# Optimization experiments

Measured on AMD Instinct MI355X. Metric: run time of the kernel, lower is better.

Reference implementation:

```python
import jax, jax.numpy as jnp
import numpy as np

HIDDEN = 1024
STATE = 16
EXPAND = 2
INNER = HIDDEN * EXPAND
BATCH, SEQ = 4, 2048


def setup_inputs() -> dict:
    key = jax.random.key(0)
    ks = jax.random.split(key, 12)
    s = 0.02
    return {
        "x": jax.random.normal(ks[0], (BATCH, SEQ, HIDDEN), jnp.float32),
        "norm_scale": jnp.ones((HIDDEN,), jnp.float32),
        "norm_bias": jnp.zeros((HIDDEN,), jnp.float32),
        "W_in": jax.random.normal(ks[1], (HIDDEN, 2 * INNER), jnp.float32) * s,
        "conv_w": jax.random.normal(ks[2], (INNER, 3), jnp.float32) * 0.3,
        "conv_b": jnp.zeros((INNER,), jnp.float32),
        "W_dt": jax.random.normal(ks[3], (INNER, INNER), jnp.float32) * s,
        "b_dt": jnp.zeros((INNER,), jnp.float32),
        "A_log": jax.random.normal(ks[4], (INNER, STATE), jnp.float32),
        "D_param": jnp.ones((INNER,), jnp.float32),
        "W_B": jax.random.normal(ks[5], (INNER, STATE), jnp.float32) * s,
        "W_C": jax.random.normal(ks[6], (INNER, STATE), jnp.float32) * s,
        "W_out": jax.random.normal(ks[7], (INNER, HIDDEN), jnp.float32) * s,
    }


def reference(x, norm_scale, norm_bias, W_in, conv_w, conv_b, W_dt, b_dt,
              A_log, D_param, W_B, W_C, W_out):
    residual = x
    # LayerNorm (eps = 1e-5, matches nn.LayerNorm default)
    mu = jnp.mean(x, axis=-1, keepdims=True)
    var = jnp.mean(jnp.square(x - mu), axis=-1, keepdims=True)
    xn = (x - mu) * jax.lax.rsqrt(var + 1e-5) * norm_scale + norm_bias

    xz = xn @ W_in                         # [B, L, 2*inner]
    xb, z = jnp.split(xz, 2, axis=-1)      # each [B, L, inner]

    # depthwise conv1d, kernel 3, padding 1 (cross-correlation as in torch)
    xp = jnp.pad(xb, ((0, 0), (1, 1), (0, 0)))
    xb = (conv_w[:, 0] * xp[:, :-2] + conv_w[:, 1] * xp[:, 1:-1]
          + conv_w[:, 2] * xp[:, 2:] + conv_b)
    xb = jax.nn.silu(xb)

    dt = jax.nn.softplus(xb @ W_dt + b_dt)  # [B, L, inner]
    A = -jnp.exp(A_log)                     # [inner, N]
    Bi = xb @ W_B                           # [B, L, N]
    Ci = xb @ W_C                           # [B, L, N]

    def step(h, inp):
        x_t, dt_t, B_t, C_t = inp           # [B,D], [B,D], [B,N], [B,N]
        A_bar = jnp.exp(dt_t[:, :, None] * A)                 # [B, D, N]
        h = A_bar * h + (dt_t * x_t)[:, :, None] * B_t[:, None, :]
        y_t = jnp.einsum('bdn,bn->bd', h, C_t)
        return h, y_t

    h0 = jnp.zeros((x.shape[0], INNER, STATE), x.dtype)
    xs = (jnp.swapaxes(xb, 0, 1), jnp.swapaxes(dt, 0, 1),
          jnp.swapaxes(Bi, 0, 1), jnp.swapaxes(Ci, 0, 1))
    _, y = jax.lax.scan(step, h0, xs)       # y: [L, B, D]
    y = jnp.swapaxes(y, 0, 1)

    y = (y + D_param * xb) * jax.nn.silu(z)
    return residual + y @ W_out
```

## Files before the change

### kernel.cpp

```cpp
#include <hip/hip_runtime.h>
#include <hip/hip_bf16.h>
#include <cstdint>
#include <cstddef>

#define B_DIM 4
#define L_DIM 2048
#define H_DIM 1024
#define D_DIM 2048
#define N_STATE 16
#define TOKENS (B_DIM * L_DIM)
#define CH 32
#define LC (L_DIM / CH)
#define NEXT 2176

typedef __bf16 bf16x8 __attribute__((ext_vector_type(8)));
typedef float f32x4 __attribute__((ext_vector_type(4)));

__device__ __forceinline__ float sigmoidf_(float x) { return 1.f / (1.f + __expf(-x)); }
__device__ __forceinline__ float softplusf_(float x) {
  return fmaxf(x, 0.f) + log1pf(__expf(-fabsf(x)));
}
__device__ __forceinline__ void gl_lds16(const void* g, void* l) {
  __builtin_amdgcn_global_load_lds(
      (const __attribute__((address_space(1))) unsigned int*)g,
      (__attribute__((address_space(3))) unsigned int*)l, 16, 0, 0);
}

__device__ __forceinline__ void do_transpose(const float* __restrict__ in,
    __hip_bfloat16* __restrict__ out, int R, int C, int c0, int r0, int t) {
  __shared__ float tile[32][33];
  int tx = t & 31, ty = t >> 5;
  for (int i = 0; i < 32; i += 8)
    tile[ty + i][tx] = in[(size_t)(r0 + ty + i) * C + c0 + tx];
  __syncthreads();
  for (int i = 0; i < 32; i += 8)
    out[(size_t)(c0 + ty + i) * R + r0 + tx] = __float2bfloat16(tile[tx][ty + i]);
}

__global__ __launch_bounds__(256) void prep_kernel(
    const float* __restrict__ x, const float* __restrict__ gamma,
    const float* __restrict__ beta, __hip_bfloat16* __restrict__ xn,
    const float* __restrict__ W_in, __hip_bfloat16* __restrict__ W_inT,
    const float* __restrict__ W_dt, __hip_bfloat16* __restrict__ Wext,
    const float* __restrict__ WB, const float* __restrict__ WC) {
  int b = blockIdx.x;
  int t = threadIdx.x;
  if (b < TOKENS) {
    const float* px = x + (size_t)b * H_DIM;
    float4 v = *(const float4*)(px + t * 4);
    float s  = v.x + v.y + v.z + v.w;
    float ss = v.x * v.x + v.y * v.y + v.z * v.z + v.w * v.w;
    for (int off = 32; off > 0; off >>= 1) {
      s  += __shfl_down(s, off);
      ss += __shfl_down(ss, off);
    }
    __shared__ float red[8];
    __shared__ float stats[2];
    int wave = t >> 6, lane = t & 63;
    if (lane == 0) { red[wave] = s; red[4 + wave] = ss; }
    __syncthreads();
    if (t == 0) {
      float S  = red[0] + red[1] + red[2] + red[3];
      float SS = red[4] + red[5] + red[6] + red[7];
      float mu = S / H_DIM;
      float var = SS / H_DIM - mu * mu;
      stats[0] = mu;
      stats[1] = rsqrtf(var + 1e-5f);
    }
    __syncthreads();
    float mu = stats[0], rstd = stats[1];
    float4 g  = *(const float4*)(gamma + t * 4);
    float4 bt = *(const float4*)(beta + t * 4);
    __hip_bfloat16* po = xn + (size_t)b * H_DIM + t * 4;
    po[0] = __float2bfloat16((v.x - mu) * rstd * g.x + bt.x);
    po[1] = __float2bfloat16((v.y - mu) * rstd * g.y + bt.y);
    po[2] = __float2bfloat16((v.z - mu) * rstd * g.z + bt.z);
    po[3] = __float2bfloat16((v.w - mu) * rstd * g.w + bt.w);
    return;
  }
  b -= TOKENS;
  if (b < 4096) {
    do_transpose(W_in, W_inT, 1024, 4096, (b & 127) * 32, (b >> 7) * 32, t);
    return;
  }
  b -= 4096;
  if (b < 4096) {
    do_transpose(W_dt, Wext, 2048, 2048, (b & 63) * 32, (b >> 6) * 32, t);
    return;
  }
  b -= 4096;
  {
    int tid = b * 256 + t;
    int c = tid & 31;
    int k0 = (tid >> 5) * 16;
    const float* W = (c < 16) ? WB : WC;
    int cc = c & 15;
    __hip_bfloat16* o = Wext + (size_t)(2048 + c) * D_DIM + k0;
    for (int kk = 0; kk < 16; ++kk)
      o[kk] = __float2bfloat16(W[(size_t)(k0 + kk) * N_STATE + cc]);
  }
}

__global__ void transpose_bf16(const float* __restrict__ in,
                               __hip_bfloat16* __restrict__ out, int R, int C) {
  __shared__ float tile[32][33];
  int c0 = blockIdx.x * 32, r0 = blockIdx.y * 32;
  int tx = threadIdx.x, ty = threadIdx.y;
  for (int i = 0; i < 32; i += 8)
    tile[ty + i][tx] = in[(size_t)(r0 + ty + i) * C + c0 + tx];
  __syncthreads();
  for (int i = 0; i < 32; i += 8)
    out[(size_t)(c0 + ty + i) * R + r0 + tx] = __float2bfloat16(tile[tx][ty + i]);
}

#define BM 128
#define BN 128
#define BK 64

template <int MODE>
__global__ __launch_bounds__(256) void gemm_bf16(
    const __hip_bfloat16* __restrict__ A, const __hip_bfloat16* __restrict__ Bt,
    void* __restrict__ C0, void* __restrict__ C1, int nsplit,
    int K, int lda, int ldb, int ldc, int gx,
    const float* __restrict__ bias, const float* __restrict__ resid) {
  __shared__ __hip_bfloat16 As[2 * BM * BK];
  __shared__ __hip_bfloat16 Bs[2 * BN * BK];
  int t = threadIdx.x;
  int bid = blockIdx.x;
  int nsup = gx << 3;
  int super = bid / nsup;
  int rem = bid - super * nsup;
  int m0 = (super * 8 + (rem & 7)) * BM;
  int n0 = (rem >> 3) * BN;

  int wave = t >> 6, lane = t & 63;
  int quad = lane >> 4, l16 = lane & 15;
  int wm = (wave >> 1) * 64, wn = (wave & 1) * 64;

  f32x4 acc[4][4] = {};

  int srow  = t >> 3;
  int cslot = t & 7;
  int cdata = cslot ^ (srow & 7);
  const __hip_bfloat16* Ag[4];
  const __hip_bfloat16* Bg[4];
  int soff[4];
#pragma unroll
  for (int j = 0; j < 4; ++j) {
    Ag[j]  = A  + (size_t)(m0 + j * 32 + srow) * lda + cdata * 8;
    Bg[j]  = Bt + (size_t)(n0 + j * 32 + srow) * ldb + cdata * 8;
    soff[j] = (j * 32 + srow) * BK + cslot * 8;
  }

  const int NT = K / BK;
#pragma unroll
  for (int j = 0; j < 4; ++j) {
    gl_lds16(Ag[j], &As[soff[j]]);
    gl_lds16(Bg[j], &Bs[soff[j]]);
  }
  asm volatile("s_waitcnt vmcnt(0)" ::: "memory");
  __builtin_amdgcn_s_barrier();

  for (int kt = 0; kt < NT; ++kt) {
    const int cur = (kt & 1) * (BM * BK);
    const int nxt = cur ^ (BM * BK);
    if (kt + 1 < NT) {
      const int k1 = (kt + 1) * BK;
#pragma unroll
      for (int j = 0; j < 4; ++j) {
        gl_lds16(Ag[j] + k1, &As[nxt + soff[j]]);
        gl_lds16(Bg[j] + k1, &Bs[nxt + soff[j]]);
      }
    }
#pragma unroll
    for (int s = 0; s < 2; ++s) {
      int cs = ((s * 4 + quad) ^ (l16 & 7)) * 8;
      bf16x8 af[4], bf_[4];
#pragma unroll
      for (int i = 0; i < 4; ++i) {
        af[i]  = *(const bf16x8*)&As[cur + (wm + i * 16 + l16) * BK + cs];
        bf_[i] = *(const bf16x8*)&Bs[cur + (wn + i * 16 + l16) * BK + cs];
      }
#pragma unroll
      for (int i = 0; i < 4; ++i)
#pragma unroll
        for (int j = 0; j < 4; ++j)
          acc[i][j] = __builtin_amdgcn_mfma_f32_16x16x32_bf16(af[i], bf_[j], acc[i][j], 0, 0, 0);
    }
    asm volatile("s_waitcnt vmcnt(0)" ::: "memory");
    __builtin_amdgcn_s_barrier();
  }

#pragma unroll
  for (int i = 0; i < 4; ++i) {
    int row0 = m0 + wm + i * 16 + quad * 4;
#pragma unroll
    for (int j = 0; j < 4; ++j) {
      int col = n0 + wn + j * 16 + l16;
      f32x4 v = acc[i][j];
      if (MODE == 0) {
#pragma unroll
        for (int r = 0; r < 4; ++r) {
          size_t idx = (size_t)(row0 + r) * ldc + col;
          ((float*)C0)[idx] = v[r] + resid[idx];
        }
      } else if (MODE == 1) {
        bool mainc = (col < nsplit);
        __hip_bfloat16* cb = mainc ? (__hip_bfloat16*)C0 : (__hip_bfloat16*)C1;
        int ccol = mainc ? col : col - nsplit;
#pragma unroll
        for (int r = 0; r < 4; ++r)
          cb[(size_t)(row0 + r) * ldc + ccol] = __float2bfloat16(v[r]);
      } else {
        if (col < nsplit) {
          float bb = bias[col];
#pragma unroll
          for (int r = 0; r < 4; ++r)
            ((__hip_bfloat16*)C0)[(size_t)(row0 + r) * ldc + col] =
                __float2bfloat16(softplusf_(v[r] + bb));
        } else {
#pragma unroll
          for (int r = 0; r < 4; ++r)
            ((float*)C1)[(size_t)(row0 + r) * 128 + (col - nsplit)] = v[r];
        }
      }
    }
  }
}

__global__ __launch_bounds__(256) void conv_silu_kernel(const __hip_bfloat16* __restrict__ xb,
    const float* __restrict__ cw, const float* __restrict__ cb,
    __hip_bfloat16* __restrict__ xbc) {
  size_t i2 = (size_t)blockIdx.x * 256 + threadIdx.x;
  int dp = (int)(i2 & (D_DIM / 2 - 1));
  size_t tok = i2 >> 10;
  int l = (int)(tok & (L_DIM - 1));
  int d = dp * 2;
  const __hip_bfloat162* base = (const __hip_bfloat162*)xb + i2;
  __hip_bfloat162 cc = base[0];
  float v0 = cw[d * 3 + 1] * __bfloat162float(cc.x) + cb[d];
  float v1 = cw[d * 3 + 4] * __bfloat162float(cc.y) + cb[d + 1];
  if (l > 0) {
    __hip_bfloat162 pm = base[-(D_DIM / 2)];
    v0 += cw[d * 3 + 0] * __bfloat162float(pm.x);
    v1 += cw[d * 3 + 3] * __bfloat162float(pm.y);
  }
  if (l < L_DIM - 1) {
    __hip_bfloat162 pp = base[D_DIM / 2];
    v0 += cw[d * 3 + 2] * __bfloat162float(pp.x);
    v1 += cw[d * 3 + 5] * __bfloat162float(pp.y);
  }
  v0 = v0 * sigmoidf_(v0);
  v1 = v1 * sigmoidf_(v1);
  __hip_bfloat162 o;
  o.x = __float2bfloat16(v0);
  o.y = __float2bfloat16(v1);
  ((__hip_bfloat162*)xbc)[i2] = o;
}

__global__ __launch_bounds__(256) void scan1_kernel(const __hip_bfloat16* __restrict__ dt,
    const __hip_bfloat16* __restrict__ xbc, const float* __restrict__ BiCi,
    const float* __restrict__ A_log, float* __restrict__ hfin,
    float* __restrict__ dtsum) {
  __shared__ float Bsh[LC * N_STATE];
  int t = threadIdx.x;
  int d = blockIdx.x * 256 + t;
  int c = blockIdx.y, b = blockIdx.z;
  size_t base = (size_t)b * L_DIM + (size_t)c * LC;
  for (int idx = t; idx < LC * 4; idx += 256) {
    int row = idx >> 2, q = idx & 3;
    ((float4*)Bsh)[row * 4 + q] = *(const float4*)&BiCi[(base + row) * 128 + q * 4];
  }
  float Aneg[N_STATE];
  {
    const float4* Ap = (const float4*)(A_log + (size_t)d * N_STATE);
#pragma unroll
    for (int q = 0; q < 4; ++q) {
      float4 av = Ap[q];
      Aneg[4 * q + 0] = -__expf(av.x);
      Aneg[4 * q + 1] = -__expf(av.y);
      Aneg[4 * q + 2] = -__expf(av.z);
      Aneg[4 * q + 3] = -__expf(av.w);
    }
  }
  __syncthreads();
  const __hip_bfloat16* dtp = dt + base * D_DIM + d;
  const __hip_bfloat16* xp = xbc + base * D_DIM + d;
  float h[N_STATE];
#pragma unroll
  for (int n = 0; n < N_STATE; ++n) h[n] = 0.f;
  float ds = 0.f;
  float dtv = __bfloat162float(dtp[0]), xv = __bfloat162float(xp[0]);
  for (int i = 0; i < LC; ++i) {
    int ip = (i < LC - 1) ? i + 1 : i;
    float dt2 = __bfloat162float(dtp[(size_t)ip * D_DIM]);
    float x2  = __bfloat162float(xp[(size_t)ip * D_DIM]);
    float dtx = dtv * xv;
    ds += dtv;
    const float4* Brow = (const float4*)&Bsh[i * N_STATE];
#pragma unroll
    for (int q = 0; q < 4; ++q) {
      float4 bv = Brow[q];
      h[4*q+0] = __expf(dtv * Aneg[4*q+0]) * h[4*q+0] + dtx * bv.x;
      h[4*q+1] = __expf(dtv * Aneg[4*q+1]) * h[4*q+1] + dtx * bv.y;
      h[4*q+2] = __expf(dtv * Aneg[4*q+2]) * h[4*q+2] + dtx * bv.z;
      h[4*q+3] = __expf(dtv * Aneg[4*q+3]) * h[4*q+3] + dtx * bv.w;
    }
    dtv = dt2; xv = x2;
  }
  float* ho = hfin + (((size_t)b * CH + c) * D_DIM + d) * N_STATE;
#pragma unroll
  for (int q = 0; q < 4; ++q) {
    float4 v; v.x = h[4*q]; v.y = h[4*q+1]; v.z = h[4*q+2]; v.w = h[4*q+3];
    ((float4*)ho)[q] = v;
  }
  dtsum[((size_t)b * CH + c) * D_DIM + d] = ds;
}

__global__ __launch_bounds__(256) void scan2_kernel(const float* __restrict__ hfin,
    const float* __restrict__ dtsum, const float* __restrict__ A_log,
    float* __restrict__ hstart) {
  int tid = blockIdx.x * 256 + threadIdx.x;
  int n = tid & 15;
  int d = (tid >> 4) & (D_DIM - 1);
  int b = tid >> 15;
  float Aneg = -__expf(A_log[d * N_STATE + n]);
  float run = 0.f;
  for (int c = 0; c < CH; ++c) {
    size_t o = (((size_t)b * CH + c) * D_DIM + d) * N_STATE + n;
    hstart[o] = run;
    run = __expf(Aneg * dtsum[((size_t)b * CH + c) * D_DIM + d]) * run + hfin[o];
  }
}

__global__ __launch_bounds__(256) void scan3_kernel(const __hip_bfloat16* __restrict__ dt,
    const __hip_bfloat16* __restrict__ xbc, const float* __restrict__ BiCi,
    const float* __restrict__ A_log,
    const float* __restrict__ hstart, const __hip_bfloat16* __restrict__ z,
    const float* __restrict__ Dp, __hip_bfloat16* __restrict__ yo) {
  __shared__ float Bsh[LC * N_STATE];
  __shared__ float Csh[LC * N_STATE];
  int t = threadIdx.x;
  int d = blockIdx.x * 256 + t;
  int c = blockIdx.y, b = blockIdx.z;
  size_t base = (size_t)b * L_DIM + (size_t)c * LC;
  for (int idx = t; idx < LC * 4; idx += 256) {
    int row = idx >> 2, q = idx & 3;
    ((float4*)Bsh)[row * 4 + q] = *(const float4*)&BiCi[(base + row) * 128 + q * 4];
    ((float4*)Csh)[row * 4 + q] = *(const float4*)&BiCi[(base + row) * 128 + 16 + q * 4];
  }
  float Aneg[N_STATE];
  {
    const float4* Ap = (const float4*)(A_log + (size_t)d * N_STATE);
#pragma unroll
    for (int q = 0; q < 4; ++q) {
      float4 av = Ap[q];
      Aneg[4 * q + 0] = -__expf(av.x);
      Aneg[4 * q + 1] = -__expf(av.y);
      Aneg[4 * q + 2] = -__expf(av.z);
      Aneg[4 * q + 3] = -__expf(av.w);
    }
  }
  float h[N_STATE];
  {
    const float4* hs = (const float4*)(hstart + (((size_t)b * CH + c) * D_DIM + d) * N_STATE);
#pragma unroll
    for (int q = 0; q < 4; ++q) {
      float4 v = hs[q];
      h[4*q] = v.x; h[4*q+1] = v.y; h[4*q+2] = v.z; h[4*q+3] = v.w;
    }
  }
  float Dv = Dp[d];
  __syncthreads();
  const __hip_bfloat16* dtp = dt + base * D_DIM + d;
  const __hip_bfloat16* xp = xbc + base * D_DIM + d;
  const __hip_bfloat16* zp = z + base * D_DIM + d;
  __hip_bfloat16* yp = yo + base * D_DIM + d;
  float dtv = __bfloat162float(dtp[0]), xv = __bfloat162float(xp[0]);
  float zv = __bfloat162float(zp[0]);
  for (int i = 0; i < LC; ++i) {
    int ip = (i < LC - 1) ? i + 1 : i;
    float dt2 = __bfloat162float(dtp[(size_t)ip * D_DIM]);
    float x2  = __bfloat162float(xp[(size_t)ip * D_DIM]);
    float z2  = __bfloat162float(zp[(size_t)ip * D_DIM]);
    float dtx = dtv * xv;
    const float4* Brow = (const float4*)&Bsh[i * N_STATE];
    const float4* Crow = (const float4*)&Csh[i * N_STATE];
    float yv = 0.f;
#pragma unroll
    for (int q = 0; q < 4; ++q) {
      float4 bv = Brow[q];
      float4 cv = Crow[q];
      h[4*q+0] = __expf(dtv * Aneg[4*q+0]) * h[4*q+0] + dtx * bv.x;
      h[4*q+1] = __expf(dtv * Aneg[4*q+1]) * h[4*q+1] + dtx * bv.y;
      h[4*q+2] = __expf(dtv * Aneg[4*q+2]) * h[4*q+2] + dtx * bv.z;
      h[4*q+3] = __expf(dtv * Aneg[4*q+3]) * h[4*q+3] + dtx * bv.w;
      yv += h[4*q+0] * cv.x + h[4*q+1] * cv.y + h[4*q+2] * cv.z + h[4*q+3] * cv.w;
    }
    float g = zv * sigmoidf_(zv);
    yp[(size_t)i * D_DIM] = __float2bfloat16((yv + Dv * xv) * g);
    dtv = dt2; xv = x2; zv = z2;
  }
}

extern "C" void kernel_launch(void* const* d_in, const int* in_sizes, int n_in,
                              void* d_out, int out_size, void* d_ws, size_t ws_size,
                              hipStream_t stream) {
  const float* x          = (const float*)d_in[0];
  const float* norm_scale = (const float*)d_in[1];
  const float* norm_bias  = (const float*)d_in[2];
  const float* W_in       = (const float*)d_in[3];
  const float* conv_w     = (const float*)d_in[4];
  const float* conv_b     = (const float*)d_in[5];
  const float* W_dt       = (const float*)d_in[6];
  const float* b_dt       = (const float*)d_in[7];
  const float* A_log      = (const float*)d_in[8];
  const float* D_param    = (const float*)d_in[9];
  const float* W_B        = (const float*)d_in[10];
  const float* W_C        = (const float*)d_in[11];
  const float* W_out      = (const float*)d_in[12];
  float* out = (float*)d_out;

  const size_t MB = 1024 * 1024;
  const size_t NEEDED = 193 * MB;
  if (ws_size < NEEDED) return;

  char* ws = (char*)d_ws;
  __hip_bfloat16* xn     = (__hip_bfloat16*)(ws);
  __hip_bfloat16* W_outT = (__hip_bfloat16*)(ws);
  __hip_bfloat16* xb     = (__hip_bfloat16*)(ws + 16 * MB);
  __hip_bfloat16* ybf    = (__hip_bfloat16*)(ws + 16 * MB);
  __hip_bfloat16* z      = (__hip_bfloat16*)(ws + 48 * MB);
  __hip_bfloat16* xbc    = (__hip_bfloat16*)(ws + 80 * MB);
  __hip_bfloat16* dtY    = (__hip_bfloat16*)(ws + 112 * MB);
  float*          BiCi   = (float*)(ws + 144 * MB);
  __hip_bfloat16* W_ext  = (__hip_bfloat16*)(ws + 148 * MB);
  float*          hstart = (float*)(ws + 158 * MB);
  float*          dtsum  = (float*)(ws + 174 * MB);
  __hip_bfloat16* W_inT  = (__hip_bfloat16*)(ws + 177 * MB);
  float*          hfin   = (float*)(ws + 177 * MB);

  prep_kernel<<<TOKENS + 4096 + 4096 + 16, 256, 0, stream>>>(
      x, norm_scale, norm_bias, xn, W_in, W_inT, W_dt, W_ext, W_B, W_C);
  gemm_bf16<1><<<(4096 / BN) * (TOKENS / BM), 256, 0, stream>>>(
      xn, W_inT, xb, z, D_DIM, H_DIM, H_DIM, H_DIM, D_DIM, 4096 / BN,
      nullptr, nullptr);
  dim3 tb(32, 8);
  transpose_bf16<<<dim3(1024 / 32, 2048 / 32), tb, 0, stream>>>(W_out, W_outT, 2048, 1024);
  conv_silu_kernel<<<(TOKENS * D_DIM / 2) / 256, 256, 0, stream>>>(xb, conv_w, conv_b, xbc);
  gemm_bf16<2><<<(NEXT / BN) * (TOKENS / BM), 256, 0, stream>>>(
      xbc, W_ext, dtY, BiCi, D_DIM, D_DIM, D_DIM, D_DIM, D_DIM, NEXT / BN,
      b_dt, nullptr);
  scan1_kernel<<<dim3(D_DIM / 256, CH, B_DIM), 256, 0, stream>>>(
      dtY, xbc, BiCi, A_log, hfin, dtsum);
  scan2_kernel<<<(B_DIM * D_DIM * N_STATE) / 256, 256, 0, stream>>>(
      hfin, dtsum, A_log, hstart);
  scan3_kernel<<<dim3(D_DIM / 256, CH, B_DIM), 256, 0, stream>>>(
      dtY, xbc, BiCi, A_log, hstart, z, D_param, ybf);
  gemm_bf16<0><<<(H_DIM / BN) * (TOKENS / BM), 256, 0, stream>>>(
      ybf, W_outT, out, nullptr, 1 << 30, D_DIM, D_DIM, D_DIM, H_DIM, H_DIM / BN,
      nullptr, x);
}
```

Baseline: 571.8 us.

## Replace three-pass chunked scan with single sequential per-state scan kernel

```diff
diff --git a/kernel.cpp b/kernel.cpp
--- a/kernel.cpp
+++ b/kernel.cpp
@@ -9,8 +9,6 @@
 #define D_DIM 2048
 #define N_STATE 16
 #define TOKENS (B_DIM * L_DIM)
-#define CH 32
-#define LC (L_DIM / CH)
 #define NEXT 2176
 
 typedef __bf16 bf16x8 __attribute__((ext_vector_type(8)));
@@ -258,148 +256,49 @@
   ((__hip_bfloat162*)xbc)[i2] = o;
 }
 
-__global__ __launch_bounds__(256) void scan1_kernel(const __hip_bfloat16* __restrict__ dt,
-    const __hip_bfloat16* __restrict__ xbc, const float* __restrict__ BiCi,
-    const float* __restrict__ A_log, float* __restrict__ hfin,
-    float* __restrict__ dtsum) {
-  __shared__ float Bsh[LC * N_STATE];
+__global__ __launch_bounds__(256) void scan_fused(
+    const __hip_bfloat16* __restrict__ dt, const __hip_bfloat16* __restrict__ xbc,
+    const float* __restrict__ BiCi, const float* __restrict__ A_log,
+    const __hip_bfloat16* __restrict__ z, const float* __restrict__ Dp,
+    __hip_bfloat16* __restrict__ yo) {
   int t = threadIdx.x;
-  int d = blockIdx.x * 256 + t;
-  int c = blockIdx.y, b = blockIdx.z;
-  size_t base = (size_t)b * L_DIM + (size_t)c * LC;
-  for (int idx = t; idx < LC * 4; idx += 256) {
-    int row = idx >> 2, q = idx & 3;
-    ((float4*)Bsh)[row * 4 + q] = *(const float4*)&BiCi[(base + row) * 128 + q * 4];
-  }
-  float Aneg[N_STATE];
-  {
-    const float4* Ap = (const float4*)(A_log + (size_t)d * N_STATE);
-#pragma unroll
-    for (int q = 0; q < 4; ++q) {
-      float4 av = Ap[q];
-      Aneg[4 * q + 0] = -__expf(av.x);
-      Aneg[4 * q + 1] = -__expf(av.y);
-      Aneg[4 * q + 2] = -__expf(av.z);
-      Aneg[4 * q + 3] = -__expf(av.w);
-    }
-  }
-  __syncthreads();
-  const __hip_bfloat16* dtp = dt + base * D_DIM + d;
-  const __hip_bfloat16* xp = xbc + base * D_DIM + d;
-  float h[N_STATE];
-#pragma unroll
-  for (int n = 0; n < N_STATE; ++n) h[n] = 0.f;
-  float ds = 0.f;
-  float dtv = __bfloat162float(dtp[0]), xv = __bfloat162float(xp[0]);
-  for (int i = 0; i < LC; ++i) {
-    int ip = (i < LC - 1) ? i + 1 : i;
-    float dt2 = __bfloat162float(dtp[(size_t)ip * D_DIM]);
-    float x2  = __bfloat162float(xp[(size_t)ip * D_DIM]);
-    float dtx = dtv * xv;
-    ds += dtv;
-    const float4* Brow = (const float4*)&Bsh[i * N_STATE];
-#pragma unroll
-    for (int q = 0; q < 4; ++q) {
-      float4 bv = Brow[q];
-      h[4*q+0] = __expf(dtv * Aneg[4*q+0]) * h[4*q+0] + dtx * bv.x;
-      h[4*q+1] = __expf(dtv * Aneg[4*q+1]) * h[4*q+1] + dtx * bv.y;
-      h[4*q+2] = __expf(dtv * Aneg[4*q+2]) * h[4*q+2] + dtx * bv.z;
-      h[4*q+3] = __expf(dtv * Aneg[4*q+3]) * h[4*q+3] + dtx * bv.w;
-    }
-    dtv = dt2; xv = x2;
-  }
-  float* ho = hfin + (((size_t)b * CH + c) * D_DIM + d) * N_STATE;
-#pragma unroll
-  for (int q = 0; q < 4; ++q) {
-    float4 v; v.x = h[4*q]; v.y = h[4*q+1]; v.z = h[4*q+2]; v.w = h[4*q+3];
-    ((float4*)ho)[q] = v;
-  }
-  dtsum[((size_t)b * CH + c) * D_DIM + d] = ds;
-}
-
-__global__ __launch_bounds__(256) void scan2_kernel(const float* __restrict__ hfin,
-    const float* __restrict__ dtsum, const float* __restrict__ A_log,
-    float* __restrict__ hstart) {
-  int tid = blockIdx.x * 256 + threadIdx.x;
-  int n = tid & 15;
-  int d = (tid >> 4) & (D_DIM - 1);
-  int b = tid >> 15;
-  float Aneg = -__expf(A_log[d * N_STATE + n]);
-  float run = 0.f;
-  for (int c = 0; c < CH; ++c) {
-    size_t o = (((size_t)b * CH + c) * D_DIM + d) * N_STATE + n;
-    hstart[o] = run;
-    run = __expf(Aneg * dtsum[((size_t)b * CH + c) * D_DIM + d]) * run + hfin[o];
-  }
-}
-
-__global__ __launch_bounds__(256) void scan3_kernel(const __hip_bfloat16* __restrict__ dt,
-    const __hip_bfloat16* __restrict__ xbc, const float* __restrict__ BiCi,
-    const float* __restrict__ A_log,
-    const float* __restrict__ hstart, const __hip_bfloat16* __restrict__ z,
-    const float* __restrict__ Dp, __hip_bfloat16* __restrict__ yo) {
-  __shared__ float Bsh[LC * N_STATE];
-  __shared__ float Csh[LC * N_STATE];
-  int t = threadIdx.x;
-  int d = blockIdx.x * 256 + t;
-  int c = blockIdx.y, b = blockIdx.z;
-  size_t base = (size_t)b * L_DIM + (size_t)c * LC;
-  for (int idx = t; idx < LC * 4; idx += 256) {
-    int row = idx >> 2, q = idx & 3;
-    ((float4*)Bsh)[row * 4 + q] = *(const float4*)&BiCi[(base + row) * 128 + q * 4];
-    ((float4*)Csh)[row * 4 + q] = *(const float4*)&BiCi[(base + row) * 128 + 16 + q * 4];
-  }
-  float Aneg[N_STATE];
-  {
-    const float4* Ap = (const float4*)(A_log + (size_t)d * N_STATE);
-#pragma unroll
-    for (int q = 0; q < 4; ++q) {
-      float4 av = Ap[q];
-      Aneg[4 * q + 0] = -__expf(av.x);
-      Aneg[4 * q + 1] = -__expf(av.y);
-      Aneg[4 * q + 2] = -__expf(av.z);
-      Aneg[4 * q + 3] = -__expf(av.w);
-    }
-  }
-  float h[N_STATE];
-  {
-    const float4* hs = (const float4*)(hstart + (((size_t)b * CH + c) * D_DIM + d) * N_STATE);
-#pragma unroll
-    for (int q = 0; q < 4; ++q) {
-      float4 v = hs[q];
-      h[4*q] = v.x; h[4*q+1] = v.y; h[4*q+2] = v.z; h[4*q+3] = v.w;
-    }
-  }
+  int n = t & 15;
+  int dl = t >> 4;
+  int b = blockIdx.x >> 7;
+  int d = ((blockIdx.x & 127) << 4) + dl;
+  float Aneg = -__expf(A_log[(size_t)d * N_STATE + n]);
   float Dv = Dp[d];
-  __syncthreads();
-  const __hip_bfloat16* dtp = dt + base * D_DIM + d;
-  const __hip_bfloat16* xp = xbc + base * D_DIM + d;
-  const __hip_bfloat16* zp = z + base * D_DIM + d;
-  __hip_bfloat16* yp = yo + base * D_DIM + d;
-  float dtv = __bfloat162float(dtp[0]), xv = __bfloat162float(xp[0]);
-  float zv = __bfloat162float(zp[0]);
-  for (int i = 0; i < LC; ++i) {
-    int ip = (i < LC - 1) ? i + 1 : i;
+  size_t tb = (size_t)b * L_DIM;
+  const __hip_bfloat16* dtp = dt + tb * D_DIM + d;
+  const __hip_bfloat16* xp  = xbc + tb * D_DIM + d;
+  const __hip_bfloat16* zp  = z + tb * D_DIM + d;
+  const float* bp = BiCi + tb * 128 + n;
+  __hip_bfloat16* yp = yo + tb * D_DIM + d;
+
+  float h = 0.f;
+  float dtv = __bfloat162float(dtp[0]);
+  float xv  = __bfloat162float(xp[0]);
+  float zv  = __bfloat162float(zp[0]);
+  float bv  = bp[0];
+  float cv  = bp[16];
+  for (int i = 0; i < L_DIM; ++i) {
+    int ip = (i < L_DIM - 1) ? i + 1 : i;
     float dt2 = __bfloat162float(dtp[(size_t)ip * D_DIM]);
     float x2  = __bfloat162float(xp[(size_t)ip * D_DIM]);
     float z2  = __bfloat162float(zp[(size_t)ip * D_DIM]);
-    float dtx = dtv * xv;
-    const float4* Brow = (const float4*)&Bsh[i * N_STATE];
-    const float4* Crow = (const float4*)&Csh[i * N_STATE];
-    float yv = 0.f;
-#pragma unroll
-    for (int q = 0; q < 4; ++q) {
-      float4 bv = Brow[q];
-      float4 cv = Crow[q];
-      h[4*q+0] = __expf(dtv * Aneg[4*q+0]) * h[4*q+0] + dtx * bv.x;
-      h[4*q+1] = __expf(dtv * Aneg[4*q+1]) * h[4*q+1] + dtx * bv.y;
-      h[4*q+2] = __expf(dtv * Aneg[4*q+2]) * h[4*q+2] + dtx * bv.z;
-      h[4*q+3] = __expf(dtv * Aneg[4*q+3]) * h[4*q+3] + dtx * bv.w;
-      yv += h[4*q+0] * cv.x + h[4*q+1] * cv.y + h[4*q+2] * cv.z + h[4*q+3] * cv.w;
-    }
-    float g = zv * sigmoidf_(zv);
-    yp[(size_t)i * D_DIM] = __float2bfloat16((yv + Dv * xv) * g);
-    dtv = dt2; xv = x2; zv = z2;
+    float b2  = bp[(size_t)ip * 128];
+    float c2  = bp[(size_t)ip * 128 + 16];
+    h = __expf(dtv * Aneg) * h + (dtv * xv) * bv;
+    float p = h * cv;
+    p += __shfl_xor(p, 1);
+    p += __shfl_xor(p, 2);
+    p += __shfl_xor(p, 4);
+    p += __shfl_xor(p, 8);
+    if (n == 0) {
+      float g = zv * sigmoidf_(zv);
+      yp[(size_t)i * D_DIM] = __float2bfloat16((p + Dv * xv) * g);
+    }
+    dtv = dt2; xv = x2; zv = z2; bv = b2; cv = c2;
   }
 }
 
@@ -435,10 +334,7 @@
   __hip_bfloat16* dtY    = (__hip_bfloat16*)(ws + 112 * MB);
   float*          BiCi   = (float*)(ws + 144 * MB);
   __hip_bfloat16* W_ext  = (__hip_bfloat16*)(ws + 148 * MB);
-  float*          hstart = (float*)(ws + 158 * MB);
-  float*          dtsum  = (float*)(ws + 174 * MB);
   __hip_bfloat16* W_inT  = (__hip_bfloat16*)(ws + 177 * MB);
-  float*          hfin   = (float*)(ws + 177 * MB);
 
   prep_kernel<<<TOKENS + 4096 + 4096 + 16, 256, 0, stream>>>(
       x, norm_scale, norm_bias, xn, W_in, W_inT, W_dt, W_ext, W_B, W_C);
@@ -451,12 +347,8 @@
   gemm_bf16<2><<<(NEXT / BN) * (TOKENS / BM), 256, 0, stream>>>(
       xbc, W_ext, dtY, BiCi, D_DIM, D_DIM, D_DIM, D_DIM, D_DIM, NEXT / BN,
       b_dt, nullptr);
-  scan1_kernel<<<dim3(D_DIM / 256, CH, B_DIM), 256, 0, stream>>>(
-      dtY, xbc, BiCi, A_log, hfin, dtsum);
-  scan2_kernel<<<(B_DIM * D_DIM * N_STATE) / 256, 256, 0, stream>>>(
-      hfin, dtsum, A_log, hstart);
-  scan3_kernel<<<dim3(D_DIM / 256, CH, B_DIM), 256, 0, stream>>>(
-      dtY, xbc, BiCi, A_log, hstart, z, D_param, ybf);
+  scan_fused<<<B_DIM * (D_DIM / 16), 256, 0, stream>>>(
+      dtY, xbc, BiCi, A_log, z, D_param, ybf);
   gemm_bf16<0><<<(H_DIM / BN) * (TOKENS / BM), 256, 0, stream>>>(
       ybf, W_outT, out, nullptr, 1 << 30, D_DIM, D_DIM, D_DIM, H_DIM, H_DIM / BN,
       nullptr, x);
```

Measured after the change: 1.223 ms. 2.14x slower.
